# Performance work log

Hardware: AMD Instinct MI355X
Metric: run time of the kernel (lower is better)

## Reference

```python
import jax, jax.numpy as jnp
import numpy as np

THRESHOLD = 0.5
NEG_POS_RATIO = 3
ALPHA = 1.0
B, P, C, O = 128, 8732, 21, 32


def xy_to_cxcy(xy):
    return jnp.concatenate([(xy[..., 2:] + xy[..., :2]) / 2, xy[..., 2:] - xy[..., :2]], axis=-1)


def cxcy_to_xy(cxcy):
    return jnp.concatenate([cxcy[..., :2] - cxcy[..., 2:] / 2, cxcy[..., :2] + cxcy[..., 2:] / 2], axis=-1)


def cxcy_to_gcxgcy(cxcy, priors_cxcy):
    g_cxcy = (cxcy[..., :2] - priors_cxcy[..., :2]) / (priors_cxcy[..., 2:] / 10.0)
    g_wh = jnp.log(cxcy[..., 2:] / priors_cxcy[..., 2:]) * 5.0
    return jnp.concatenate([g_cxcy, g_wh], axis=-1)


def find_jaccard_overlap(set1, set2):
    # set1: [O,4] xy, set2: [P,4] xy -> [O,P]
    lo = jnp.maximum(set1[:, None, :2], set2[None, :, :2])
    hi = jnp.minimum(set1[:, None, 2:], set2[None, :, 2:])
    inter = jnp.prod(jnp.clip(hi - lo, 0.0), axis=-1)
    a1 = jnp.prod(set1[:, 2:] - set1[:, :2], axis=-1)
    a2 = jnp.prod(set2[:, 2:] - set2[:, :2], axis=-1)
    union = a1[:, None] + a2[None, :] - inter
    return inter / union


def setup_inputs() -> dict:
    key = jax.random.key(0)
    k0, k1, k2, k3, k4, k5, k6 = jax.random.split(key, 7)
    predicted_locs = jax.random.normal(k0, (B, P, 4), jnp.float32)
    predicted_scores = jax.random.normal(k1, (B, P, C), jnp.float32)
    centers = jax.random.uniform(k2, (B, O, 2), jnp.float32, 0.2, 0.8)
    sizes = jax.random.uniform(k3, (B, O, 2), jnp.float32, 0.05, 0.3)
    boxes = jnp.concatenate([centers - sizes / 2, centers + sizes / 2], axis=-1)
    labels = jax.random.randint(k4, (B, O), 0, C)
    p_c = jax.random.uniform(k5, (P, 2), jnp.float32, 0.05, 0.95)
    p_wh = jax.random.uniform(k6, (P, 2), jnp.float32, 0.05, 0.5)
    priors_cxcy = jnp.concatenate([p_c, p_wh], axis=-1)
    return {"predicted_locs": predicted_locs, "predicted_scores": predicted_scores,
            "boxes": boxes, "labels": labels, "priors_cxcy": priors_cxcy}


def reference(predicted_locs, predicted_scores, boxes, labels, priors_cxcy):
    priors_xy = cxcy_to_xy(priors_cxcy)

    def match_one(boxes_i, labels_i):
        overlap = find_jaccard_overlap(boxes_i, priors_xy)           # [O,P]
        overlap_for_each_prior = jnp.max(overlap, axis=0)            # [P]
        object_for_each_prior = jnp.argmax(overlap, axis=0)          # [P]
        prior_for_each_object = jnp.argmax(overlap, axis=1)          # [O]
        object_for_each_prior = object_for_each_prior.at[prior_for_each_object].set(jnp.arange(O))
        overlap_for_each_prior = overlap_for_each_prior.at[prior_for_each_object].set(1.0)
        label_for_each_prior = labels_i[object_for_each_prior]
        label_for_each_prior = jnp.where(overlap_for_each_prior < THRESHOLD, 0, label_for_each_prior)
        true_locs_i = cxcy_to_gcxgcy(xy_to_cxcy(boxes_i[object_for_each_prior]), priors_cxcy)
        return label_for_each_prior, true_locs_i

    true_classes, true_locs = jax.vmap(match_one)(boxes, labels)     # [B,P], [B,P,4]

    positive = true_classes != 0                                     # [B,P]
    n_positives = jnp.sum(positive, axis=1)                          # [B]
    n_pos_total = jnp.sum(n_positives)

    # L1Loss (mean over selected positive elements, 4 per prior)
    abs_diff = jnp.abs(predicted_locs - true_locs)                   # [B,P,4]
    loc_loss = jnp.sum(abs_diff * positive[..., None]) / (n_pos_total.astype(jnp.float32) * 4.0)

    # per-element cross-entropy
    log_p = jax.nn.log_softmax(predicted_scores, axis=-1)            # [B,P,C]
    conf_loss_all = -jnp.take_along_axis(log_p, true_classes[..., None], axis=-1)[..., 0]  # [B,P]

    conf_loss_pos_sum = jnp.sum(jnp.where(positive, conf_loss_all, 0.0))
    conf_loss_neg = jnp.where(positive, 0.0, conf_loss_all)
    conf_loss_neg_sorted = -jnp.sort(-conf_loss_neg, axis=1)         # descending
    n_hard = NEG_POS_RATIO * n_positives                             # [B]
    hard_mask = jnp.arange(P)[None, :] < n_hard[:, None]             # [B,P]
    conf_loss_hard_neg_sum = jnp.sum(jnp.where(hard_mask, conf_loss_neg_sorted, 0.0))

    conf_loss = (conf_loss_hard_neg_sum + conf_loss_pos_sum) / n_pos_total.astype(jnp.float32)
    return conf_loss + ALPHA * loc_loss
```

## Files before the change

### kernel.cpp

```cpp
#include <hip/hip_runtime.h>
#include <hip/hip_bf16.h>

#define NB 128
#define NP 8732
#define NO 32
#define NC 21
#define NCH 8
#define CH 1152


__global__ __launch_bounds__(256) void k_obj(const float* __restrict__ boxes,
                                             const float* __restrict__ priors,
                                             unsigned long long* __restrict__ packed2,
                                             int* __restrict__ npos,
                                             double* __restrict__ accb,
                                             int* __restrict__ flag) {
    __shared__ float4 spri[CH];
    __shared__ float4 sbox[NO];
    const int ch = blockIdx.x, b = blockIdx.y, tid = threadIdx.x;
    const int lane = tid & 63, wid = tid >> 6;
    const int pbeg = ch * CH;
    const int n = min(CH, NP - pbeg);

    if (ch == 0) {
        if (tid == 0) npos[b] = 0;
        if (tid >= 1 && tid <= 3) accb[b * 3 + (tid - 1)] = 0.0;
        if (b == 0 && tid == 4) *flag = 0;
    }
    if (tid < NO) sbox[tid] = ((const float4*)boxes)[b * NO + tid];
    for (int i = tid; i < n; i += 256) {
        float4 pr = ((const float4*)priors)[pbeg + i];
        spri[i] = make_float4(pr.x - pr.z * 0.5f, pr.y - pr.w * 0.5f,
                              pr.x + pr.z * 0.5f, pr.y + pr.w * 0.5f);
    }
    __syncthreads();

#pragma unroll
    for (int oo = 0; oo < 8; ++oo) {
        const int o = wid * 8 + oo;
        float4 bx = sbox[o];
        float a1 = (bx.z - bx.x) * (bx.w - bx.y);
        unsigned long long pk = 0ull;
        for (int i = lane; i < n; i += 64) {
            float4 pr = spri[i];
            float lx = fmaxf(bx.x, pr.x), ly = fmaxf(bx.y, pr.y);
            float hx = fminf(bx.z, pr.z), hy = fminf(bx.w, pr.w);
            float iw = fmaxf(hx - lx, 0.0f), ih = fmaxf(hy - ly, 0.0f);
            float inter = iw * ih;
            float pa = (pr.z - pr.x) * (pr.w - pr.y);
            float iou = inter / (a1 + pa - inter);
            unsigned long long k2 =
                ((unsigned long long)__float_as_uint(iou) << 32) |
                (unsigned long long)(0xFFFFFFFFu - (unsigned)(pbeg + i));
            if (k2 > pk) pk = k2;
        }
        for (int s = 32; s > 0; s >>= 1) {
            unsigned long long t = __shfl_xor(pk, s, 64);
            if (t > pk) pk = t;
        }
        if (lane == 0) packed2[(b * NO + o) * NCH + ch] = pk;
    }
}

__global__ __launch_bounds__(256) void k_loss(const float* __restrict__ plocs,
                                              const float* __restrict__ scores,
                                              const float* __restrict__ boxes,
                                              const int* __restrict__ labels,
                                              const float* __restrict__ priors,
                                              const unsigned long long* __restrict__ packed2,
                                              float* __restrict__ confneg,
                                              int* __restrict__ npos,
                                              double* __restrict__ accb) {
    __shared__ float srow[256 * NC];
    __shared__ float4 sbox[NO];
    __shared__ int sfp[NO];
    __shared__ int slab[NO];
    const int b = blockIdx.y, tid = threadIdx.x;
    const int p0 = blockIdx.x * 256;
    const int cnt = min(256, NP - p0);

    {
        unsigned long long key = packed2[b * (NO * NCH) + tid];
#pragma unroll
        for (int s = 1; s < 8; s <<= 1) {
            unsigned long long t = __shfl_xor(key, s, 64);
            if (t > key) key = t;
        }
        if ((tid & 7) == 0)
            sfp[tid >> 3] = (int)(0xFFFFFFFFu - (unsigned)(key & 0xFFFFFFFFull));
    }
    if (tid < NO) {
        sbox[tid] = ((const float4*)boxes)[b * NO + tid];
        slab[tid] = labels[b * NO + tid];
    }
    const int nf4 = cnt * NC / 4;
    const float4* src4 = (const float4*)(scores + ((size_t)b * NP + p0) * NC);
    for (int i = tid; i < nf4; i += 256) ((float4*)srow)[i] = src4[i];
    __syncthreads();

    float posconf = 0.0f, locpart = 0.0f;
    int isp = 0;

    if (tid < cnt) {
        const int p = p0 + tid;
        float4 pr = ((const float4*)priors)[p];
        float px1 = pr.x - pr.z * 0.5f, py1 = pr.y - pr.w * 0.5f;
        float px2 = pr.x + pr.z * 0.5f, py2 = pr.y + pr.w * 0.5f;
        float pa = (px2 - px1) * (py2 - py1);

        float bestv = -1.0f;
        int besto = 0;
#pragma unroll
        for (int o = 0; o < NO; ++o) {
            float4 bx = sbox[o];
            float a1 = (bx.z - bx.x) * (bx.w - bx.y);
            float lx = fmaxf(bx.x, px1), ly = fmaxf(bx.y, py1);
            float hx = fminf(bx.z, px2), hy = fminf(bx.w, py2);
            float iw = fmaxf(hx - lx, 0.0f), ih = fmaxf(hy - ly, 0.0f);
            float inter = iw * ih;
            float iou = inter / (a1 + pa - inter);
            if (iou > bestv) { bestv = iou; besto = o; }
        }
        int ovr = -1;
#pragma unroll
        for (int o = 0; o < NO; ++o)
            if (sfp[o] == p) ovr = o;

        int obj, matched;
        if (ovr >= 0) { obj = ovr; matched = 1; }
        else          { obj = besto; matched = (bestv >= 0.5f) ? 1 : 0; }
        int lbl = matched ? slab[obj] : 0;

        const float* s = srow + tid * NC;
        float m = s[0];
#pragma unroll
        for (int c = 1; c < NC; ++c) m = fmaxf(m, s[c]);
        float sum = 0.0f;
#pragma unroll
        for (int c = 0; c < NC; ++c) sum += __expf(s[c] - m);
        float conf = m + __logf(sum) - s[lbl];

        if (lbl != 0) {
            isp = 1;
            posconf = conf;
            float4 bx = sbox[obj];
            float cx = (bx.x + bx.z) * 0.5f, cy = (bx.y + bx.w) * 0.5f;
            float w = bx.z - bx.x, h = bx.w - bx.y;
            float gx = (cx - pr.x) / (pr.z * 0.1f);
            float gy = (cy - pr.y) / (pr.w * 0.1f);
            float gw = __logf(w / pr.z) * 5.0f;
            float gh = __logf(h / pr.w) * 5.0f;
            float4 pl = ((const float4*)plocs)[(size_t)b * NP + p];
            locpart = fabsf(pl.x - gx) + fabsf(pl.y - gy) +
                      fabsf(pl.z - gw) + fabsf(pl.w - gh);
        }
        confneg[(size_t)b * NP + p] = isp ? 0.0f : conf;
    }

    for (int s = 32; s > 0; s >>= 1) {
        posconf += __shfl_xor(posconf, s, 64);
        locpart += __shfl_xor(locpart, s, 64);
        isp     += __shfl_xor(isp, s, 64);
    }
    __shared__ float w0[4], w1[4];
    __shared__ int wc[4];
    int wid = tid >> 6, lane = tid & 63;
    if (lane == 0) { w0[wid] = posconf; w1[wid] = locpart; wc[wid] = isp; }
    __syncthreads();
    if (tid == 0) {
        atomicAdd(&npos[b], wc[0] + wc[1] + wc[2] + wc[3]);
        atomicAdd(&accb[b * 3 + 0], (double)(w0[0] + w0[1] + w0[2] + w0[3]));
        atomicAdd(&accb[b * 3 + 1], (double)(w1[0] + w1[1] + w1[2] + w1[3]));
    }
}

__global__ __launch_bounds__(1024) void k_topk_final(const float* __restrict__ confneg,
                                                     const int* __restrict__ npos,
                                                     double* __restrict__ accb,
                                                     int* __restrict__ flag,
                                                     float* __restrict__ out) {
    __shared__ int   si[2][16];
    __shared__ double sd[16];
    __shared__ int   slast;
    const int tid = threadIdx.x, b = blockIdx.x;
    const int lane = tid & 63, wid = tid >> 6;

    const float* src = confneg + (size_t)b * NP;
    float val[9];
#pragma unroll
    for (int j = 0; j < 9; ++j) {
        int i = tid + j * 1024;
        val[j] = (i < NP) ? src[i] : 0.0f;
    }
    int k = npos[b] * 3;
    if (k > NP) k = NP;

    if (k > 0) {
        unsigned T = 0;
        for (int bit = 30; bit >= 0; --bit) {
            unsigned cand = T | (1u << bit);
            int cnt = 0;
#pragma unroll
            for (int j = 0; j < 9; ++j)
                cnt += (__float_as_uint(val[j]) >= cand) ? 1 : 0;
            for (int s = 32; s > 0; s >>= 1) cnt += __shfl_xor(cnt, s, 64);
            if (lane == 0) si[bit & 1][wid] = cnt;
            __syncthreads();
            int tot = 0;
#pragma unroll
            for (int w = 0; w < 16; ++w) tot += si[bit & 1][w];
            if (tot >= k) T = cand;
        }
        int cgt = 0;
        double sgt = 0.0;
#pragma unroll
        for (int j = 0; j < 9; ++j) {
            unsigned u = __float_as_uint(val[j]);
            if (u > T) { cgt++; sgt += (double)val[j]; }
        }
        for (int s = 32; s > 0; s >>= 1) {
            cgt += __shfl_xor(cgt, s, 64);
            sgt += __shfl_xor(sgt, s, 64);
        }
        if (lane == 0) { si[0][wid] = cgt; sd[wid] = sgt; }
        __syncthreads();
        if (tid == 0) {
            int cg = 0; double sg = 0.0;
            for (int w = 0; w < 16; ++w) { cg += si[0][w]; sg += sd[w]; }
            accb[b * 3 + 2] = sg + (double)(k - cg) * (double)__uint_as_float(T);
        }
    }

    __threadfence();
    if (tid == 0) slast = (atomicAdd(flag, 1) == NB - 1) ? 1 : 0;
    __syncthreads();
    if (slast) {
        __threadfence();
        double pc = 0, lc = 0, hn = 0, nn = 0;
        if (tid < NB) {
            pc = accb[tid * 3 + 0];
            lc = accb[tid * 3 + 1];
            hn = accb[tid * 3 + 2];
            nn = (double)npos[tid];
        }
        if (tid < 128) {
            for (int s = 32; s > 0; s >>= 1) {
                pc += __shfl_xor(pc, s, 64);
                lc += __shfl_xor(lc, s, 64);
                hn += __shfl_xor(hn, s, 64);
                nn += __shfl_xor(nn, s, 64);
            }
            if (lane == 0) { sd[wid * 4 + 0] = pc; sd[wid * 4 + 1] = lc;
                             sd[wid * 4 + 2] = hn; sd[wid * 4 + 3] = nn; }
        }
        __syncthreads();
        if (tid == 0) {
            double P  = sd[0] + sd[4];
            double L  = sd[1] + sd[5];
            double H  = sd[2] + sd[6];
            double NT = sd[3] + sd[7];
            out[0] = (float)((H + P) / NT + L / (NT * 4.0));
        }
    }
}

extern "C" void kernel_launch(void* const* d_in, const int* in_sizes, int n_in,
                              void* d_out, int out_size, void* d_ws, size_t ws_size,
                              hipStream_t stream) {
    const float* plocs  = (const float*)d_in[0];
    const float* scores = (const float*)d_in[1];
    const float* boxes  = (const float*)d_in[2];
    const int*   labels = (const int*)d_in[3];
    const float* priors = (const float*)d_in[4];
    float* out = (float*)d_out;

    char* ws = (char*)d_ws;
    unsigned long long* packed2 = (unsigned long long*)ws;
    int*    npos    = (int*)(ws + 262144);
    double* accb    = (double*)(ws + 262656);
    int*    flag    = (int*)(ws + 265728);
    float*  confneg = (float*)(ws + 265984);

    hipLaunchKernelGGL(k_obj, dim3(NCH, NB), dim3(256), 0, stream,
                       boxes, priors, packed2, npos, accb, flag);
    hipLaunchKernelGGL(k_loss, dim3((NP + 255) / 256, NB), dim3(256), 0, stream,
                       plocs, scores, boxes, labels, priors, packed2, confneg, npos, accb);
    hipLaunchKernelGGL(k_topk_final, dim3(NB), dim3(1024), 0, stream,
                       confneg, npos, accb, flag, out);
}
```

Measured before the change: 268.5 us.

## Compute per-prior best object in match kernel and fuse top-k into loss kernel

The match kernel now loops over priors with 8 boxes held in registers. It computes the per-object best prior and the per-prior best object together, combining the four waves with shared-memory 64-bit atomicMax, and writes a packed code array. The loss kernel reads that code instead of recomputing 32 IoUs per prior. The last block per image, elected by a per-image counter, runs the hard-negative threshold search, which removes the third kernel launch. The cost is an extra global code array write and read, shared atomics, and a serialized 256-thread top-k tail per image instead of a 1024-thread block.

```diff
diff --git a/kernel.cpp b/kernel.cpp
--- a/kernel.cpp
+++ b/kernel.cpp
@@ -7,15 +7,19 @@
 #define NC 21
 #define NCH 8
 #define CH 1152
-
-
-__global__ __launch_bounds__(256) void k_obj(const float* __restrict__ boxes,
-                                             const float* __restrict__ priors,
-                                             unsigned long long* __restrict__ packed2,
-                                             int* __restrict__ npos,
-                                             double* __restrict__ accb,
-                                             int* __restrict__ flag) {
+#define NPB ((NP + 255) / 256)
+
+
+__global__ __launch_bounds__(256) void k_match(const float* __restrict__ boxes,
+                                               const float* __restrict__ priors,
+                                               unsigned long long* __restrict__ packed2,
+                                               int* __restrict__ code,
+                                               int* __restrict__ npos,
+                                               double* __restrict__ accb,
+                                               int* __restrict__ flag,
+                                               int* __restrict__ imgcnt) {
     __shared__ float4 spri[CH];
+    __shared__ unsigned long long skey[CH];
     __shared__ float4 sbox[NO];
     const int ch = blockIdx.x, b = blockIdx.y, tid = threadIdx.x;
     const int lane = tid & 63, wid = tid >> 6;
@@ -25,40 +29,63 @@
     if (ch == 0) {
         if (tid == 0) npos[b] = 0;
         if (tid >= 1 && tid <= 3) accb[b * 3 + (tid - 1)] = 0.0;
-        if (b == 0 && tid == 4) *flag = 0;
+        if (tid == 4) imgcnt[b] = 0;
+        if (b == 0 && tid == 5) *flag = 0;
     }
     if (tid < NO) sbox[tid] = ((const float4*)boxes)[b * NO + tid];
     for (int i = tid; i < n; i += 256) {
         float4 pr = ((const float4*)priors)[pbeg + i];
         spri[i] = make_float4(pr.x - pr.z * 0.5f, pr.y - pr.w * 0.5f,
                               pr.x + pr.z * 0.5f, pr.y + pr.w * 0.5f);
-    }
-    __syncthreads();
-
+        skey[i] = 0ull;
+    }
+    __syncthreads();
+
+    float bxx[8], bxy[8], bxz[8], bxw[8], a1[8];
 #pragma unroll
     for (int oo = 0; oo < 8; ++oo) {
-        const int o = wid * 8 + oo;
-        float4 bx = sbox[o];
-        float a1 = (bx.z - bx.x) * (bx.w - bx.y);
-        unsigned long long pk = 0ull;
-        for (int i = lane; i < n; i += 64) {
-            float4 pr = spri[i];
-            float lx = fmaxf(bx.x, pr.x), ly = fmaxf(bx.y, pr.y);
-            float hx = fminf(bx.z, pr.z), hy = fminf(bx.w, pr.w);
+        float4 bx = sbox[wid * 8 + oo];
+        bxx[oo] = bx.x; bxy[oo] = bx.y; bxz[oo] = bx.z; bxw[oo] = bx.w;
+        a1[oo] = (bx.z - bx.x) * (bx.w - bx.y);
+    }
+    unsigned long long okey[8] = {0ull,0ull,0ull,0ull,0ull,0ull,0ull,0ull};
+
+    for (int i = lane; i < n; i += 64) {
+        float4 pr = spri[i];
+        float pa = (pr.z - pr.x) * (pr.w - pr.y);
+        const unsigned long long inv_p =
+            (unsigned long long)(0xFFFFFFFFu - (unsigned)(pbeg + i));
+        unsigned long long pkey = 0ull;
+#pragma unroll
+        for (int oo = 0; oo < 8; ++oo) {
+            float lx = fmaxf(bxx[oo], pr.x), ly = fmaxf(bxy[oo], pr.y);
+            float hx = fminf(bxz[oo], pr.z), hy = fminf(bxw[oo], pr.w);
             float iw = fmaxf(hx - lx, 0.0f), ih = fmaxf(hy - ly, 0.0f);
             float inter = iw * ih;
-            float pa = (pr.z - pr.x) * (pr.w - pr.y);
-            float iou = inter / (a1 + pa - inter);
-            unsigned long long k2 =
-                ((unsigned long long)__float_as_uint(iou) << 32) |
-                (unsigned long long)(0xFFFFFFFFu - (unsigned)(pbeg + i));
-            if (k2 > pk) pk = k2;
-        }
+            float iou = inter / (a1[oo] + pa - inter);
+            unsigned long long base = ((unsigned long long)__float_as_uint(iou) << 32);
+            unsigned long long ko = base | inv_p;
+            if (ko > okey[oo]) okey[oo] = ko;
+            unsigned long long kp = base | (unsigned)(NO - 1 - (wid * 8 + oo));
+            if (kp > pkey) pkey = kp;
+        }
+        atomicMax(&skey[i], pkey);
+    }
+#pragma unroll
+    for (int oo = 0; oo < 8; ++oo) {
+        unsigned long long pk = okey[oo];
         for (int s = 32; s > 0; s >>= 1) {
             unsigned long long t = __shfl_xor(pk, s, 64);
             if (t > pk) pk = t;
         }
-        if (lane == 0) packed2[(b * NO + o) * NCH + ch] = pk;
+        if (lane == 0) packed2[(b * NO + wid * 8 + oo) * NCH + ch] = pk;
+    }
+    __syncthreads();
+    for (int i = tid; i < n; i += 256) {
+        unsigned long long k = skey[i];
+        int o = NO - 1 - (int)(unsigned)(k & 0xFFFFFFFFull);
+        float bv = __uint_as_float((unsigned)(k >> 32));
+        code[(size_t)b * NP + pbeg + i] = o | (bv >= 0.5f ? 256 : 0);
     }
 }
 
@@ -68,16 +95,26 @@
                                               const int* __restrict__ labels,
                                               const float* __restrict__ priors,
                                               const unsigned long long* __restrict__ packed2,
+                                              const int* __restrict__ code,
                                               float* __restrict__ confneg,
                                               int* __restrict__ npos,
-                                              double* __restrict__ accb) {
+                                              double* __restrict__ accb,
+                                              int* __restrict__ flag,
+                                              int* __restrict__ imgcnt,
+                                              float* __restrict__ out) {
     __shared__ float srow[256 * NC];
     __shared__ float4 sbox[NO];
     __shared__ int sfp[NO];
     __shared__ int slab[NO];
+    __shared__ float w0[4], w1[4];
+    __shared__ int wc[4];
+    __shared__ int si[2][4];
+    __shared__ double sd[8];
+    __shared__ int sElect, sFinal;
     const int b = blockIdx.y, tid = threadIdx.x;
     const int p0 = blockIdx.x * 256;
     const int cnt = min(256, NP - p0);
+    const int wid = tid >> 6, lane = tid & 63;
 
     {
         unsigned long long key = packed2[b * (NO * NCH) + tid];
@@ -103,32 +140,14 @@
 
     if (tid < cnt) {
         const int p = p0 + tid;
-        float4 pr = ((const float4*)priors)[p];
-        float px1 = pr.x - pr.z * 0.5f, py1 = pr.y - pr.w * 0.5f;
-        float px2 = pr.x + pr.z * 0.5f, py2 = pr.y + pr.w * 0.5f;
-        float pa = (px2 - px1) * (py2 - py1);
-
-        float bestv = -1.0f;
-        int besto = 0;
-#pragma unroll
-        for (int o = 0; o < NO; ++o) {
-            float4 bx = sbox[o];
-            float a1 = (bx.z - bx.x) * (bx.w - bx.y);
-            float lx = fmaxf(bx.x, px1), ly = fmaxf(bx.y, py1);
-            float hx = fminf(bx.z, px2), hy = fminf(bx.w, py2);
-            float iw = fmaxf(hx - lx, 0.0f), ih = fmaxf(hy - ly, 0.0f);
-            float inter = iw * ih;
-            float iou = inter / (a1 + pa - inter);
-            if (iou > bestv) { bestv = iou; besto = o; }
-        }
+        int cd = code[(size_t)b * NP + p];
+        int obj = cd & 255;
+        int matched = (cd >> 8) & 1;
         int ovr = -1;
 #pragma unroll
         for (int o = 0; o < NO; ++o)
             if (sfp[o] == p) ovr = o;
-
-        int obj, matched;
         if (ovr >= 0) { obj = ovr; matched = 1; }
-        else          { obj = besto; matched = (bestv >= 0.5f) ? 1 : 0; }
         int lbl = matched ? slab[obj] : 0;
 
         const float* s = srow + tid * NC;
@@ -143,6 +162,7 @@
         if (lbl != 0) {
             isp = 1;
             posconf = conf;
+            float4 pr = ((const float4*)priors)[p];
             float4 bx = sbox[obj];
             float cx = (bx.x + bx.z) * 0.5f, cy = (bx.y + bx.w) * 0.5f;
             float w = bx.z - bx.x, h = bx.w - bx.y;
@@ -162,104 +182,97 @@
         locpart += __shfl_xor(locpart, s, 64);
         isp     += __shfl_xor(isp, s, 64);
     }
-    __shared__ float w0[4], w1[4];
-    __shared__ int wc[4];
-    int wid = tid >> 6, lane = tid & 63;
     if (lane == 0) { w0[wid] = posconf; w1[wid] = locpart; wc[wid] = isp; }
     __syncthreads();
     if (tid == 0) {
         atomicAdd(&npos[b], wc[0] + wc[1] + wc[2] + wc[3]);
         atomicAdd(&accb[b * 3 + 0], (double)(w0[0] + w0[1] + w0[2] + w0[3]));
         atomicAdd(&accb[b * 3 + 1], (double)(w1[0] + w1[1] + w1[2] + w1[3]));
-    }
-}
-
-__global__ __launch_bounds__(1024) void k_topk_final(const float* __restrict__ confneg,
-                                                     const int* __restrict__ npos,
-                                                     double* __restrict__ accb,
-                                                     int* __restrict__ flag,
-                                                     float* __restrict__ out) {
-    __shared__ int   si[2][16];
-    __shared__ double sd[16];
-    __shared__ int   slast;
-    const int tid = threadIdx.x, b = blockIdx.x;
-    const int lane = tid & 63, wid = tid >> 6;
-
-    const float* src = confneg + (size_t)b * NP;
-    float val[9];
-#pragma unroll
-    for (int j = 0; j < 9; ++j) {
-        int i = tid + j * 1024;
-        val[j] = (i < NP) ? src[i] : 0.0f;
-    }
-    int k = npos[b] * 3;
-    if (k > NP) k = NP;
-
-    if (k > 0) {
-        unsigned T = 0;
-        for (int bit = 30; bit >= 0; --bit) {
-            unsigned cand = T | (1u << bit);
-            int cnt = 0;
-#pragma unroll
-            for (int j = 0; j < 9; ++j)
-                cnt += (__float_as_uint(val[j]) >= cand) ? 1 : 0;
-            for (int s = 32; s > 0; s >>= 1) cnt += __shfl_xor(cnt, s, 64);
-            if (lane == 0) si[bit & 1][wid] = cnt;
+        __threadfence();
+        int t = atomicAdd(&imgcnt[b], 1);
+        sElect = (t == NPB - 1) ? 1 : 0;
+    }
+    __syncthreads();
+
+    if (sElect) {
+        __threadfence();
+        const float* src = confneg + (size_t)b * NP;
+        float val[35];
+#pragma unroll
+        for (int j = 0; j < 35; ++j) {
+            int i = tid + j * 256;
+            val[j] = (i < NP) ? src[i] : 0.0f;
+        }
+        int k = npos[b] * 3;
+        if (k > NP) k = NP;
+        if (k > 0) {
+            unsigned T = 0;
+            for (int bit = 30; bit >= 0; --bit) {
+                unsigned cand = T | (1u << bit);
+                int c2 = 0;
+#pragma unroll
+                for (int j = 0; j < 35; ++j)
+                    c2 += (__float_as_uint(val[j]) >= cand) ? 1 : 0;
+                for (int s = 32; s > 0; s >>= 1) c2 += __shfl_xor(c2, s, 64);
+                if (lane == 0) si[bit & 1][wid] = c2;
+                __syncthreads();
+                int tot = si[bit & 1][0] + si[bit & 1][1] + si[bit & 1][2] + si[bit & 1][3];
+                if (tot >= k) T = cand;
+            }
+            int cgt = 0;
+            double sgt = 0.0;
+#pragma unroll
+            for (int j = 0; j < 35; ++j) {
+                unsigned u = __float_as_uint(val[j]);
+                if (u > T) { cgt++; sgt += (double)val[j]; }
+            }
+            for (int s = 32; s > 0; s >>= 1) {
+                cgt += __shfl_xor(cgt, s, 64);
+                sgt += __shfl_xor(sgt, s, 64);
+            }
             __syncthreads();
-            int tot = 0;
-#pragma unroll
-            for (int w = 0; w < 16; ++w) tot += si[bit & 1][w];
-            if (tot >= k) T = cand;
-        }
-        int cgt = 0;
-        double sgt = 0.0;
-#pragma unroll
-        for (int j = 0; j < 9; ++j) {
-            unsigned u = __float_as_uint(val[j]);
-            if (u > T) { cgt++; sgt += (double)val[j]; }
-        }
-        for (int s = 32; s > 0; s >>= 1) {
-            cgt += __shfl_xor(cgt, s, 64);
-            sgt += __shfl_xor(sgt, s, 64);
-        }
-        if (lane == 0) { si[0][wid] = cgt; sd[wid] = sgt; }
+            if (lane == 0) { si[0][wid] = cgt; sd[wid] = sgt; }
+            __syncthreads();
+            if (tid == 0) {
+                int cg = si[0][0] + si[0][1] + si[0][2] + si[0][3];
+                double sg = sd[0] + sd[1] + sd[2] + sd[3];
+                accb[b * 3 + 2] = sg + (double)(k - cg) * (double)__uint_as_float(T);
+            }
+        }
+
+        if (tid == 0) {
+            __threadfence();
+            int t2 = atomicAdd(flag, 1);
+            sFinal = (t2 == NB - 1) ? 1 : 0;
+        }
         __syncthreads();
-        if (tid == 0) {
-            int cg = 0; double sg = 0.0;
-            for (int w = 0; w < 16; ++w) { cg += si[0][w]; sg += sd[w]; }
-            accb[b * 3 + 2] = sg + (double)(k - cg) * (double)__uint_as_float(T);
-        }
-    }
-
-    __threadfence();
-    if (tid == 0) slast = (atomicAdd(flag, 1) == NB - 1) ? 1 : 0;
-    __syncthreads();
-    if (slast) {
-        __threadfence();
-        double pc = 0, lc = 0, hn = 0, nn = 0;
-        if (tid < NB) {
-            pc = accb[tid * 3 + 0];
-            lc = accb[tid * 3 + 1];
-            hn = accb[tid * 3 + 2];
-            nn = (double)npos[tid];
-        }
-        if (tid < 128) {
-            for (int s = 32; s > 0; s >>= 1) {
-                pc += __shfl_xor(pc, s, 64);
-                lc += __shfl_xor(lc, s, 64);
-                hn += __shfl_xor(hn, s, 64);
-                nn += __shfl_xor(nn, s, 64);
-            }
-            if (lane == 0) { sd[wid * 4 + 0] = pc; sd[wid * 4 + 1] = lc;
-                             sd[wid * 4 + 2] = hn; sd[wid * 4 + 3] = nn; }
-        }
-        __syncthreads();
-        if (tid == 0) {
-            double P  = sd[0] + sd[4];
-            double L  = sd[1] + sd[5];
-            double H  = sd[2] + sd[6];
-            double NT = sd[3] + sd[7];
-            out[0] = (float)((H + P) / NT + L / (NT * 4.0));
+        if (sFinal) {
+            __threadfence();
+            double pc = 0, lc = 0, hn = 0, nn = 0;
+            if (tid < NB) {
+                pc = accb[tid * 3 + 0];
+                lc = accb[tid * 3 + 1];
+                hn = accb[tid * 3 + 2];
+                nn = (double)npos[tid];
+            }
+            if (tid < 128) {
+                for (int s = 32; s > 0; s >>= 1) {
+                    pc += __shfl_xor(pc, s, 64);
+                    lc += __shfl_xor(lc, s, 64);
+                    hn += __shfl_xor(hn, s, 64);
+                    nn += __shfl_xor(nn, s, 64);
+                }
+                if (lane == 0) { sd[wid * 4 + 0] = pc; sd[wid * 4 + 1] = lc;
+                                 sd[wid * 4 + 2] = hn; sd[wid * 4 + 3] = nn; }
+            }
+            __syncthreads();
+            if (tid == 0) {
+                double P  = sd[0] + sd[4];
+                double L  = sd[1] + sd[5];
+                double H  = sd[2] + sd[6];
+                double NT = sd[3] + sd[7];
+                out[0] = (float)((H + P) / NT + L / (NT * 4.0));
+            }
         }
     }
 }
@@ -279,12 +292,13 @@
     int*    npos    = (int*)(ws + 262144);
     double* accb    = (double*)(ws + 262656);
     int*    flag    = (int*)(ws + 265728);
-    float*  confneg = (float*)(ws + 265984);
-
-    hipLaunchKernelGGL(k_obj, dim3(NCH, NB), dim3(256), 0, stream,
-                       boxes, priors, packed2, npos, accb, flag);
-    hipLaunchKernelGGL(k_loss, dim3((NP + 255) / 256, NB), dim3(256), 0, stream,
-                       plocs, scores, boxes, labels, priors, packed2, confneg, npos, accb);
-    hipLaunchKernelGGL(k_topk_final, dim3(NB), dim3(1024), 0, stream,
-                       confneg, npos, accb, flag, out);
+    int*    imgcnt  = (int*)(ws + 265984);
+    int*    code    = (int*)(ws + 266496);
+    float*  confneg = (float*)(ws + 266496 + (size_t)NB * NP * 4);
+
+    hipLaunchKernelGGL(k_match, dim3(NCH, NB), dim3(256), 0, stream,
+                       boxes, priors, packed2, code, npos, accb, flag, imgcnt);
+    hipLaunchKernelGGL(k_loss, dim3(NPB, NB), dim3(256), 0, stream,
+                       plocs, scores, boxes, labels, priors, packed2, code,
+                       confneg, npos, accb, flag, imgcnt, out);
 }
```

New measurement: 505.4 us. 88.2% more time.
